# Optimization experiments

Hardware: AMD Instinct MI355X
Metric: run time of the kernel (lower is better)

Reference implementation:

```python
import jax, jax.numpy as jnp
import numpy as np

B = 16384
D_IN, HID = 4, 128
N1, N2, N3 = 32, 8, 128   # capsule counts: 32 -> 8 -> 128
D_COV, D_CAP = 1, 4
N_ITERS = 3
EPS = 1e-5


def heinsen_routing(a_inp, mu_inp, W, Bb, beta_use, beta_ign):
    """Heinsen (2019) capsule routing.
    a_inp: [b, n_inp] activations; mu_inp: [b, n_inp, d_cov, d_inp] capsules.
    W: [n_inp or 1, n_out, d_inp, d_out]; Bb: [n_out, d_cov, d_out];
    beta_use/beta_ign: [n_out].
    """
    n_inp = a_inp.shape[1]
    W = jnp.broadcast_to(W, (n_inp,) + W.shape[1:])
    n_out = W.shape[1]
    # votes V: [b, n_inp, n_out, d_cov, d_out]
    V = jnp.einsum('ijdh,bicd->bijch', W, mu_inp) + Bb
    f_a = jax.nn.sigmoid(a_inp)[..., None]  # [b, n_inp, 1]
    a_out = mu_out = sig2_out = None
    for it in range(N_ITERS):
        if it == 0:
            R = jnp.full(V.shape[:3], 1.0 / n_out, V.dtype)
        else:
            diff2 = (V - mu_out[:, None]) ** 2
            log_p = (-0.5 * diff2 / sig2_out[:, None]
                     - 0.5 * jnp.log(2.0 * np.pi * sig2_out[:, None])).sum((-2, -1))
            R = jax.nn.softmax(jax.nn.log_sigmoid(a_out)[:, None, :] + log_p, axis=-1)
        D_use = f_a * R                       # [b, n_inp, n_out]
        D_ign = f_a - D_use
        a_out = beta_use * D_use.sum(1) - beta_ign * D_ign.sum(1)  # [b, n_out]
        inv = 1.0 / (D_use.sum(1) + EPS)
        mu_out = jnp.einsum('bij,bijch->bjch', D_use, V) * inv[..., None, None]
        sig2_out = jnp.einsum('bij,bijch->bjch', D_use, (V - mu_out[:, None]) ** 2) * inv[..., None, None] + EPS
    return a_out, mu_out, sig2_out


def setup_inputs() -> dict:
    key = jax.random.key(0)
    ks = jax.random.split(key, 16)
    rn = lambda k, s, sc=1.0: (jax.random.normal(k, s) * sc).astype(jnp.float32)
    inp = rn(ks[0], (B, D_IN))
    W1 = rn(ks[1], (HID, D_IN), 1.0 / np.sqrt(D_IN)); b1 = jnp.zeros((HID,), jnp.float32)
    Wa = rn(ks[2], (HID, HID), 1.0 / np.sqrt(HID)); ba = jnp.zeros((HID,), jnp.float32)
    Wv = rn(ks[3], (N1, HID), 1.0 / np.sqrt(HID)); bv = jnp.zeros((N1,), jnp.float32)
    R1_W = rn(ks[4], (1, N2, D_CAP, D_CAP), 1.0 / D_CAP)   # n_inp not fixed -> shared W
    R1_B = rn(ks[5], (N2, D_COV, D_CAP), 0.1)
    R1_bu = rn(ks[6], (N2,), 0.1); R1_bi = rn(ks[7], (N2,), 0.1)
    R2_W = rn(ks[8], (N2, N3, D_CAP, D_CAP), 1.0 / D_CAP)
    R2_B = rn(ks[9], (N3, D_COV, D_CAP), 0.1)
    R2_bu = rn(ks[10], (N3,), 0.1); R2_bi = rn(ks[11], (N3,), 0.1)
    sub_w = rn(ks[12], (2, D_IN))  # SubNetwork weight, 2 actions x 4 input feats
    return dict(inp=inp, W1=W1, b1=b1, Wa=Wa, ba=ba, Wv=Wv, bv=bv,
                R1_W=R1_W, R1_B=R1_B, R1_bu=R1_bu, R1_bi=R1_bi,
                R2_W=R2_W, R2_B=R2_B, R2_bu=R2_bu, R2_bi=R2_bi, sub_w=sub_w)


def reference(inp, W1, b1, Wa, ba, Wv, bv, R1_W, R1_B, R1_bu, R1_bi,
              R2_W, R2_B, R2_bu, R2_bi, sub_w):
    x = jax.nn.relu(inp @ W1.T + b1)                                  # [B,128]
    action_caps = (x @ Wa.T + ba).reshape(-1, N1, D_COV, D_CAP)        # [B,32,1,4]
    state_caps = x @ Wv.T + bv                                         # [B,32]
    a, mu, _ = heinsen_routing(state_caps, action_caps, R1_W, R1_B, R1_bu, R1_bi)
    a, mu, _ = heinsen_routing(a, mu, R2_W, R2_B, R2_bu, R2_bi)        # [B,128], [B,128,1,4]
    value = a.max(axis=1)                                              # critic value [B]
    idx = jnp.argmax(a, axis=1)                                        # [B]
    sel = jnp.take_along_axis(mu, idx[:, None, None, None], axis=1)[:, 0, 0, :]  # [B,4]
    action_prob = jax.nn.softmax(sel, axis=-1)
    k1, k2, k3 = jax.random.split(jax.random.key(42), 3)
    sub_action = jax.random.categorical(k1, jnp.log(action_prob + 1e-20), axis=-1)  # [B]
    eps = jax.random.normal(k2, (inp.shape[0],) + sub_w.shape)          # [B,2,4]
    new_w = jnp.clip(jnp.where(sub_action[:, None, None] == 0, sub_w * eps, sub_w / eps), -1.0, 1.0)
    final = jnp.einsum('bi,boi->bo', inp, new_w)                       # [B,2]
    out_probs = jax.nn.softmax(final, axis=-1)
    action = jax.random.categorical(k3, jnp.log(out_probs + 1e-20), axis=-1)  # [B]
    log_prob = jnp.take_along_axis(jnp.log(out_probs + 1e-20), action[:, None], axis=1)[:, 0]
    return action, log_prob, value
```

## Files before the change

kernel.cpp:

```cpp
#include <hip/hip_runtime.h>
#include <cstdint>

#define BB 16384
#define EPSR 1e-5f
#define TWO_PI 6.2831855f

struct U2 { uint32_t x, y; };

__host__ __device__ constexpr uint32_t rotl32(uint32_t x, int r) {
  return (x << r) | (x >> (32 - r));
}

__host__ __device__ constexpr U2 tf2x32(uint32_t k0, uint32_t k1, uint32_t x0, uint32_t x1) {
  uint32_t ks0 = k0, ks1 = k1, ks2 = k0 ^ k1 ^ 0x1BD11BDAu;
  x0 += ks0; x1 += ks1;
  x0 += x1; x1 = rotl32(x1, 13); x1 ^= x0;
  x0 += x1; x1 = rotl32(x1, 15); x1 ^= x0;
  x0 += x1; x1 = rotl32(x1, 26); x1 ^= x0;
  x0 += x1; x1 = rotl32(x1, 6);  x1 ^= x0;
  x0 += ks1; x1 += ks2 + 1u;
  x0 += x1; x1 = rotl32(x1, 17); x1 ^= x0;
  x0 += x1; x1 = rotl32(x1, 29); x1 ^= x0;
  x0 += x1; x1 = rotl32(x1, 16); x1 ^= x0;
  x0 += x1; x1 = rotl32(x1, 24); x1 ^= x0;
  x0 += ks2; x1 += ks0 + 2u;
  x0 += x1; x1 = rotl32(x1, 13); x1 ^= x0;
  x0 += x1; x1 = rotl32(x1, 15); x1 ^= x0;
  x0 += x1; x1 = rotl32(x1, 26); x1 ^= x0;
  x0 += x1; x1 = rotl32(x1, 6);  x1 ^= x0;
  x0 += ks0; x1 += ks1 + 3u;
  x0 += x1; x1 = rotl32(x1, 17); x1 ^= x0;
  x0 += x1; x1 = rotl32(x1, 29); x1 ^= x0;
  x0 += x1; x1 = rotl32(x1, 16); x1 ^= x0;
  x0 += x1; x1 = rotl32(x1, 24); x1 ^= x0;
  x0 += ks1; x1 += ks2 + 4u;
  x0 += x1; x1 = rotl32(x1, 13); x1 ^= x0;
  x0 += x1; x1 = rotl32(x1, 15); x1 ^= x0;
  x0 += x1; x1 = rotl32(x1, 26); x1 ^= x0;
  x0 += x1; x1 = rotl32(x1, 6);  x1 ^= x0;
  x0 += ks2; x1 += ks0 + 5u;
  return U2{x0, x1};
}

static_assert(tf2x32(0u, 0u, 0u, 2u).x == 4146024105u, "threefry KAT A.x");
static_assert(tf2x32(0u, 0u, 0u, 2u).y == 2718843009u, "threefry KAT A.y");
static_assert(tf2x32(0u, 0u, 1u, 3u).x == 967050713u,  "threefry KAT B.x");
static_assert(tf2x32(0u, 0u, 1u, 3u).y == 1272950319u, "threefry KAT B.y");

constexpr U2 KK1 = tf2x32(0u, 42u, 0u, 0u);
constexpr U2 KK2 = tf2x32(0u, 42u, 0u, 1u);
constexpr U2 KK3 = tf2x32(0u, 42u, 0u, 2u);

__device__ __forceinline__ uint32_t rbits(uint32_t ka, uint32_t kb, uint32_t n) {
  U2 r = tf2x32(ka, kb, 0u, n);
  return r.x ^ r.y;
}

__device__ __forceinline__ float u01f(uint32_t bits) {
  return __uint_as_float((bits >> 9) | 0x3F800000u) - 1.0f;
}

__device__ __forceinline__ float gumbel_from(uint32_t bits) {
  #pragma clang fp contract(off)
  const float tiny = 1.17549435e-38f;
  float f = u01f(bits);
  float u = f * 1.0f + tiny;
  u = fmaxf(tiny, u);
  return -logf(-logf(u));
}

__device__ __forceinline__ float normal_from(uint32_t bits) {
  #pragma clang fp contract(off)
  const float lo = -0.99999994f;
  float f = u01f(bits);
  float u = f * 2.0f + lo;
  u = fmaxf(lo, u);
  float w = -log1pf(-(u * u));
  float p;
  if (w < 5.0f) {
    w = w - 2.5f;
    p = 2.81022636e-08f;
    p = 3.43273939e-07f  + p * w;
    p = -3.5233877e-06f  + p * w;
    p = -4.39150654e-06f + p * w;
    p = 0.00021858087f   + p * w;
    p = -0.00125372503f  + p * w;
    p = -0.00417768164f  + p * w;
    p = 0.246640727f     + p * w;
    p = 1.50140941f      + p * w;
  } else {
    w = sqrtf(w) - 3.0f;
    p = -0.000200214257f;
    p = 0.000100950558f  + p * w;
    p = 0.00134934322f   + p * w;
    p = -0.00367342844f  + p * w;
    p = 0.00573950773f   + p * w;
    p = -0.0076224613f   + p * w;
    p = 0.00943887047f   + p * w;
    p = 1.00167406f      + p * w;
    p = 2.83297682f      + p * w;
  }
  return 1.41421356f * (p * u);
}

__device__ __forceinline__ float frcp(float x)  { return __builtin_amdgcn_rcpf(x); }
__device__ __forceinline__ float fexp(float x)  { return __expf(x); }
__device__ __forceinline__ float flog(float x)  { return __logf(x); }
__device__ __forceinline__ float fsig(float x)  { return frcp(1.0f + fexp(-x)); }
__device__ __forceinline__ float flogsig(float x) {
  return fminf(x, 0.0f) - flog(1.0f + fexp(-fabsf(x)));
}

template<int CTRL>
__device__ __forceinline__ float fdpp(float x) {
  return __int_as_float(__builtin_amdgcn_update_dpp(
      0, __float_as_int(x), CTRL, 0xF, 0xF, true));
}
template<int CTRL>
__device__ __forceinline__ int idpp(int x) {
  return __builtin_amdgcn_update_dpp(0, x, CTRL, 0xF, 0xF, true);
}
__device__ __forceinline__ float fswz16(float x) {
  return __int_as_float(__builtin_amdgcn_ds_swizzle(__float_as_int(x), 0x401F));
}
__device__ __forceinline__ int iswz16(int x) {
  return __builtin_amdgcn_ds_swizzle(x, 0x401F);
}

__device__ __forceinline__ float redh_sum(float x) {
  x += fdpp<0xB1>(x);
  x += fdpp<0x4E>(x);
  return x;
}
__device__ __forceinline__ float red8j_sum(float x) {
  x += fdpp<0x124>(x);
  x += fdpp<0x128>(x);
  x += fswz16(x);
  return x;
}
__device__ __forceinline__ float red64_sum(float x) {
  x += fdpp<0xB1>(x);
  x += fdpp<0x4E>(x);
  x += fdpp<0x124>(x);
  x += fdpp<0x128>(x);
  x += fswz16(x);
  x += __shfl_xor(x, 32);
  return x;
}

__global__ __launch_bounds__(256) void feat_kernel(
    const float* __restrict__ inp, const float* __restrict__ W1, const float* __restrict__ b1,
    const float* __restrict__ Wa, const float* __restrict__ ba,
    const float* __restrict__ Wv, const float* __restrict__ bv,
    float* __restrict__ feat) {
  __shared__ float xs[16][129];
  const int t = threadIdx.x;
  const int bl = t & 15;
  const int og = t >> 4;
  const int b = blockIdx.x * 16 + bl;
  const float4 in4 = *reinterpret_cast<const float4*>(inp + b * 4);
  #pragma unroll
  for (int kk = 0; kk < 8; ++kk) {
    int k = og * 8 + kk;
    float s = in4.x * W1[k * 4 + 0] + in4.y * W1[k * 4 + 1] +
              in4.z * W1[k * 4 + 2] + in4.w * W1[k * 4 + 3];
    s += b1[k];
    xs[bl][k] = fmaxf(s, 0.0f);
  }
  __syncthreads();
  #pragma unroll
  for (int pass = 0; pass < 2; ++pass) {
    const int o0 = og * 10 + pass * 5;
    const float* rr0; const float* rr1; const float* rr2;
    const float* rr3; const float* rr4;
    float bs[5];
    {
      int oo = o0 + 0; rr0 = (oo < 128) ? Wa + oo * 128 : Wv + (oo - 128) * 128;
      bs[0] = (oo < 128) ? ba[oo] : bv[oo - 128];
      oo = o0 + 1; rr1 = (oo < 128) ? Wa + oo * 128 : Wv + (oo - 128) * 128;
      bs[1] = (oo < 128) ? ba[oo] : bv[oo - 128];
      oo = o0 + 2; rr2 = (oo < 128) ? Wa + oo * 128 : Wv + (oo - 128) * 128;
      bs[2] = (oo < 128) ? ba[oo] : bv[oo - 128];
      oo = o0 + 3; rr3 = (oo < 128) ? Wa + oo * 128 : Wv + (oo - 128) * 128;
      bs[3] = (oo < 128) ? ba[oo] : bv[oo - 128];
      oo = o0 + 4; rr4 = (oo < 128) ? Wa + oo * 128 : Wv + (oo - 128) * 128;
      bs[4] = (oo < 128) ? ba[oo] : bv[oo - 128];
    }
    float s0 = 0.f, s1 = 0.f, s2 = 0.f, s3 = 0.f, s4 = 0.f;
    #pragma unroll 8
    for (int k = 0; k < 128; ++k) {
      float xv = xs[bl][k];
      s0 += rr0[k] * xv;
      s1 += rr1[k] * xv;
      s2 += rr2[k] * xv;
      s3 += rr3[k] * xv;
      s4 += rr4[k] * xv;
    }
    float* fo = feat + b * 160 + o0;
    fo[0] = s0 + bs[0]; fo[1] = s1 + bs[1]; fo[2] = s2 + bs[2];
    fo[3] = s3 + bs[3]; fo[4] = s4 + bs[4];
  }
}

__global__ __launch_bounds__(128, 4) void route_kernel(
    const float* __restrict__ feat,
    const float* __restrict__ R1W, const float* __restrict__ R1B,
    const float* __restrict__ R1bu, const float* __restrict__ R1bi,
    const float* __restrict__ R2W, const float* __restrict__ R2B,
    const float* __restrict__ R2bu, const float* __restrict__ R2bi,
    const float* __restrict__ inp, const float* __restrict__ sub_w,
    float* __restrict__ out) {
  const int lane = threadIdx.x & 63;
  const int w = threadIdx.x >> 6;
  const int b = blockIdx.x;
  const float* fb = feat + b * 160;

  __shared__ float4 r1a[3][2][32];
  __shared__ float  r1g[2][2][32];
  __shared__ float  exS[2][2][8];
  __shared__ float s_av[2];
  __shared__ int   s_ai[2];
  __shared__ float s_mu[2][4];

  const int c = lane & 31;
  const int ihalf = lane >> 5;
  const int q = w * 2 + ihalf;
  const int j1 = c >> 2, h1 = c & 3;
  const float w1r0 = R1W[(j1 * 4 + 0) * 4 + h1];
  const float w1r1 = R1W[(j1 * 4 + 1) * 4 + h1];
  const float w1r2 = R1W[(j1 * 4 + 2) * 4 + h1];
  const float w1r3 = R1W[(j1 * 4 + 3) * 4 + h1];
  const float bc1 = R1B[j1 * 4 + h1];
  const float bu1 = R1bu[j1], bi1 = R1bi[j1];

  const float sfm = fsig(fb[128 + w * 16 + (lane & 15)]);

  float v1[8], f0[8];
  #pragma unroll
  for (int ii = 0; ii < 8; ++ii) {
    int i = q * 8 + ii;
    float4 m = *reinterpret_cast<const float4*>(fb + i * 4);
    v1[ii] = w1r0 * m.x + w1r1 * m.y + w1r2 * m.z + w1r3 * m.w + bc1;
    f0[ii] = __shfl(sfm, ihalf * 8 + ii);
  }

  float a1, mu1, sig1;
  {
    float S = 0.f, Sg = 0.f, num = 0.f;
    #pragma unroll
    for (int ii = 0; ii < 8; ++ii) {
      float D = f0[ii] * 0.125f;
      S += D;
      Sg += (f0[ii] - D);
      num += D * v1[ii];
    }
    S += __shfl_xor(S, 32); Sg += __shfl_xor(Sg, 32); num += __shfl_xor(num, 32);
    if (lane < 32) r1a[0][w][c] = make_float4(S, Sg, num, 0.f);
    __syncthreads();
    float4 o = r1a[0][w ^ 1][c];
    S += o.x; Sg += o.y; num += o.z;
    a1 = bu1 * S - bi1 * Sg;
    float inv = frcp(S + EPSR);
    mu1 = num * inv;
    float sg = 0.f;
    #pragma unroll
    for (int ii = 0; ii < 8; ++ii) {
      float D = f0[ii] * 0.125f;
      float tt = v1[ii] - mu1;
      sg += D * (tt * tt);
    }
    sg += __shfl_xor(sg, 32);
    if (lane < 32) r1g[0][w][c] = sg;
    __syncthreads();
    sg += r1g[0][w ^ 1][c];
    sig1 = sg * inv + EPSR;
  }
  #pragma unroll
  for (int it = 1; it < 3; ++it) {
    const bool needsig = (it == 1);
    float lsig = flogsig(a1);
    float lt1 = -(0.5f * flog(TWO_PI * sig1));
    float nhis = -0.5f * frcp(sig1);
    float Darr[8];
    float S = 0.f, Sg = 0.f, num = 0.f;
    #pragma unroll
    for (int ii = 0; ii < 8; ++ii) {
      float tt = v1[ii] - mu1;
      float lp = (tt * tt) * nhis + lt1;
      lp = redh_sum(lp);
      float logit = lsig + lp;
      float e = fexp(logit);
      float den = red8j_sum(e);
      float D = f0[ii] * (e * frcp(den));
      Darr[ii] = D;
      S += D;
      Sg += (f0[ii] - D);
      num += D * v1[ii];
    }
    S += __shfl_xor(S, 32); Sg += __shfl_xor(Sg, 32); num += __shfl_xor(num, 32);
    if (lane < 32) r1a[it][w][c] = make_float4(S, Sg, num, 0.f);
    __syncthreads();
    float4 o = r1a[it][w ^ 1][c];
    S += o.x; Sg += o.y; num += o.z;
    a1 = bu1 * S - bi1 * Sg;
    float inv = frcp(S + EPSR);
    mu1 = num * inv;
    if (needsig) {
      float sg = 0.f;
      #pragma unroll
      for (int ii = 0; ii < 8; ++ii) {
        float tt = v1[ii] - mu1;
        sg += Darr[ii] * (tt * tt);
      }
      sg += __shfl_xor(sg, 32);
      if (lane < 32) r1g[1][w][c] = sg;
      __syncthreads();
      sg += r1g[1][w ^ 1][c];
      sig1 = sg * inv + EPSR;
    }
  }

  const float sa = fsig(__shfl(a1, (lane & 7) * 4));
  float f1[8];
  #pragma unroll
  for (int i = 0; i < 8; ++i) f1[i] = __shfl(sa, i);

  const int j = w * 64 + lane;
  const float4 b4 = *reinterpret_cast<const float4*>(R2B + j * 4);
  const float bb2[4] = {b4.x, b4.y, b4.z, b4.w};
  const float bu2 = R2bu[j], bi2 = R2bi[j];

  float v2[8][4];
  #pragma unroll
  for (int i = 0; i < 8; ++i) {
    float m0 = __shfl(mu1, i * 4 + 0);
    float m1 = __shfl(mu1, i * 4 + 1);
    float m2 = __shfl(mu1, i * 4 + 2);
    float m3 = __shfl(mu1, i * 4 + 3);
    const float4* wp = reinterpret_cast<const float4*>(R2W + i * 2048 + j * 16);
    float4 c0 = wp[0], c1 = wp[1], c2 = wp[2], c3 = wp[3];
    v2[i][0] = m0 * c0.x + m1 * c1.x + m2 * c2.x + m3 * c3.x + bb2[0];
    v2[i][1] = m0 * c0.y + m1 * c1.y + m2 * c2.y + m3 * c3.y + bb2[1];
    v2[i][2] = m0 * c0.z + m1 * c1.z + m2 * c2.z + m3 * c3.z + bb2[2];
    v2[i][3] = m0 * c0.w + m1 * c1.w + m2 * c2.w + m3 * c3.w + bb2[3];
  }

  float a2, mu[4], sg[4];
  {
    float S = 0.f, Sg = 0.f;
    #pragma unroll
    for (int i = 0; i < 8; ++i) {
      float D = f1[i] * 0.0078125f;
      S += D;
      Sg += (f1[i] - D);
    }
    a2 = bu2 * S - bi2 * Sg;
    float inv = frcp(S + EPSR);
    #pragma unroll
    for (int h = 0; h < 4; ++h) {
      float n = 0.f;
      #pragma unroll
      for (int i = 0; i < 8; ++i) n += (f1[i] * 0.0078125f) * v2[i][h];
      mu[h] = n * inv;
    }
    #pragma unroll
    for (int h = 0; h < 4; ++h) {
      float s2 = 0.f;
      #pragma unroll
      for (int i = 0; i < 8; ++i) {
        float D = f1[i] * 0.0078125f;
        float t = v2[i][h] - mu[h];
        s2 += D * (t * t);
      }
      sg[h] = s2 * inv + EPSR;
    }
  }

  float e[8], stw[8];
  #pragma unroll
  for (int it = 1; it < 3; ++it) {
    const bool needsig = (it == 1);
    float lsig = flogsig(a2);
    float lt[4], is[4];
    #pragma unroll
    for (int h = 0; h < 4; ++h) {
      lt[h] = -(0.5f * flog(TWO_PI * sg[h]));
      is[h] = -0.5f * frcp(sg[h]);
    }
    #pragma unroll
    for (int i = 0; i < 8; ++i) {
      float lp = 0.f;
      #pragma unroll
      for (int h = 0; h < 4; ++h) {
        float t = v2[i][h] - mu[h];
        lp += (t * t) * is[h] + lt[h];
      }
      float l = lsig + lp;
      e[i] = fexp(l);
      stw[i] = red64_sum(e[i]);
    }
    if (lane == 0) {
      #pragma unroll
      for (int i = 0; i < 8; ++i) exS[it - 1][w][i] = stw[i];
    }
    __syncthreads();
    float D[8];
    float SA = 0.f, SgS = 0.f;
    float n[4] = {0.f, 0.f, 0.f, 0.f};
    #pragma unroll
    for (int i = 0; i < 8; ++i) {
      float Stot = stw[i] + exS[it - 1][w ^ 1][i];
      float Dv = f1[i] * (e[i] * frcp(Stot));
      D[i] = Dv;
      SA += Dv;
      SgS += (f1[i] - Dv);
      #pragma unroll
      for (int h = 0; h < 4; ++h) n[h] += Dv * v2[i][h];
    }
    a2 = bu2 * SA - bi2 * SgS;
    float inv = frcp(SA + EPSR);
    #pragma unroll
    for (int h = 0; h < 4; ++h) mu[h] = n[h] * inv;
    if (needsig) {
      #pragma unroll
      for (int h = 0; h < 4; ++h) {
        float s2 = 0.f;
        #pragma unroll
        for (int i = 0; i < 8; ++i) {
          float t = v2[i][h] - mu[h];
          s2 += D[i] * (t * t);
        }
        sg[h] = s2 * inv + EPSR;
      }
    }
  }

  float bv = a2; int bj = j;
  {
    float ov; int oj;
    ov = fdpp<0xB1>(bv);  oj = idpp<0xB1>(bj);
    if (ov > bv || (ov == bv && oj < bj)) { bv = ov; bj = oj; }
    ov = fdpp<0x4E>(bv);  oj = idpp<0x4E>(bj);
    if (ov > bv || (ov == bv && oj < bj)) { bv = ov; bj = oj; }
    ov = fdpp<0x124>(bv); oj = idpp<0x124>(bj);
    if (ov > bv || (ov == bv && oj < bj)) { bv = ov; bj = oj; }
    ov = fdpp<0x128>(bv); oj = idpp<0x128>(bj);
    if (ov > bv || (ov == bv && oj < bj)) { bv = ov; bj = oj; }
    ov = fswz16(bv);      oj = iswz16(bj);
    if (ov > bv || (ov == bv && oj < bj)) { bv = ov; bj = oj; }
    ov = __shfl_xor(bv, 32); oj = __shfl_xor(bj, 32);
    if (ov > bv || (ov == bv && oj < bj)) { bv = ov; bj = oj; }
  }
  if (lane == 0) { s_av[w] = bv; s_ai[w] = bj; }
  if (j == bj) {
    s_mu[w][0] = mu[0]; s_mu[w][1] = mu[1]; s_mu[w][2] = mu[2]; s_mu[w][3] = mu[3];
  }
  __syncthreads();

  if (w == 0) {
    float av0 = s_av[0], av1 = s_av[1];
    float value; int winw;
    if (av1 > av0) { value = av1; winw = 1; }
    else           { value = av0; winw = 0; }
    float sel[4] = {s_mu[winw][0], s_mu[winw][1], s_mu[winw][2], s_mu[winw][3]};

    float gu, no;
    {
      uint32_t ka, kb, nn;
      if (lane < 4)       { ka = KK1.x; kb = KK1.y; nn = (uint32_t)(b * 4 + lane); }
      else if (lane < 12) { ka = KK2.x; kb = KK2.y; nn = (uint32_t)(b * 8 + (lane - 4)); }
      else                { ka = KK3.x; kb = KK3.y; nn = (uint32_t)(b * 2 + (lane & 1)); }
      uint32_t bits = rbits(ka, kb, nn);
      gu = gumbel_from(bits);
      no = normal_from(bits);
    }
    const float g0 = __shfl(gu, 0), g1 = __shfl(gu, 1);
    const float g2 = __shfl(gu, 2), g3 = __shfl(gu, 3);
    float ep[8];
    #pragma unroll
    for (int i = 0; i < 8; ++i) ep[i] = __shfl(no, 4 + i);
    const float q0 = __shfl(gu, 12), q1 = __shfl(gu, 13);

    float mx = fmaxf(fmaxf(sel[0], sel[1]), fmaxf(sel[2], sel[3]));
    float ex[4], sesum = 0.f;
    #pragma unroll
    for (int cc = 0; cc < 4; ++cc) { ex[cc] = fexp(sel[cc] - mx); sesum += ex[cc]; }
    float rs0 = frcp(sesum);
    float lg1[4];
    #pragma unroll
    for (int cc = 0; cc < 4; ++cc) lg1[cc] = flog(ex[cc] * rs0 + 1e-20f);

    float sc0 = g0 + lg1[0], sc1 = g1 + lg1[1];
    float sc2 = g2 + lg1[2], sc3 = g3 + lg1[3];
    int sub_action = 0;
    float bestsc = sc0;
    if (sc1 > bestsc) { bestsc = sc1; sub_action = 1; }
    if (sc2 > bestsc) { bestsc = sc2; sub_action = 2; }
    if (sc3 > bestsc) { bestsc = sc3; sub_action = 3; }

    float4 ib4 = *reinterpret_cast<const float4*>(inp + b * 4);
    float inb[4] = {ib4.x, ib4.y, ib4.z, ib4.w};
    float fin[2];
    #pragma unroll
    for (int o = 0; o < 2; ++o) {
      float acc = 0.f;
      #pragma unroll
      for (int i2 = 0; i2 < 4; ++i2) {
        float eps = ep[o * 4 + i2];
        float sw = sub_w[o * 4 + i2];
        float nw = (sub_action == 0) ? sw * eps : sw / eps;
        nw = fminf(fmaxf(nw, -1.0f), 1.0f);
        acc += inb[i2] * nw;
      }
      fin[o] = acc;
    }

    float mx2 = fmaxf(fin[0], fin[1]);
    float e0 = fexp(fin[0] - mx2), e1 = fexp(fin[1] - mx2);
    float rsum = frcp(e0 + e1);
    float lgp0 = flog(e0 * rsum + 1e-20f);
    float lgp1 = flog(e1 * rsum + 1e-20f);
    float s0 = q0 + lgp0;
    float s1 = q1 + lgp1;
    int action = (s1 > s0) ? 1 : 0;
    float log_prob = action ? lgp1 : lgp0;

    if (lane == 0) {
      out[b] = (float)action;
      out[BB + b] = log_prob;
      out[2 * BB + b] = value;
    }
  }
}

extern "C" void kernel_launch(void* const* d_in, const int* in_sizes, int n_in,
                              void* d_out, int out_size, void* d_ws, size_t ws_size,
                              hipStream_t stream) {
  const float* inp  = (const float*)d_in[0];
  const float* W1   = (const float*)d_in[1];
  const float* b1   = (const float*)d_in[2];
  const float* Wa   = (const float*)d_in[3];
  const float* ba   = (const float*)d_in[4];
  const float* Wv   = (const float*)d_in[5];
  const float* bv   = (const float*)d_in[6];
  const float* R1W  = (const float*)d_in[7];
  const float* R1B  = (const float*)d_in[8];
  const float* R1bu = (const float*)d_in[9];
  const float* R1bi = (const float*)d_in[10];
  const float* R2W  = (const float*)d_in[11];
  const float* R2B  = (const float*)d_in[12];
  const float* R2bu = (const float*)d_in[13];
  const float* R2bi = (const float*)d_in[14];
  const float* sub_w= (const float*)d_in[15];
  float* out = (float*)d_out;
  float* feat = (float*)d_ws;

  feat_kernel<<<BB / 16, 256, 0, stream>>>(inp, W1, b1, Wa, ba, Wv, bv, feat);
  route_kernel<<<BB, 128, 0, stream>>>(feat, R1W, R1B, R1bu, R1bi,
                                       R2W, R2B, R2bu, R2bi, inp, sub_w, out);
}
```

Baseline: 163.6 us.

## Retile feature kernel, fold log-prob constants into exp2, stage mu via LDS

The feature kernel now handles 64 batch rows per block, with a wave-uniform output group and the 160 outputs split across 4 blocks. This is meant to reuse each weight-row load across more rows, at the cost of recomputing the first layer in every quarter block. In both routing stages the per-dimension log-normal constants and log-sigmoid are folded into a single pre-scaled constant, and exp is swapped for a raw exp2 to trim VALU work. The stage-2 broadcast of mu1 and the sigmoid activations now goes through shared memory with float4 reads instead of many shuffles, which adds one extra barrier.

```diff
diff --git a/kernel.cpp b/kernel.cpp
--- a/kernel.cpp
+++ b/kernel.cpp
@@ -4,6 +4,7 @@
 #define BB 16384
 #define EPSR 1e-5f
 #define TWO_PI 6.2831855f
+#define L2E 1.44269504f
 
 struct U2 { uint32_t x, y; };
 
@@ -106,6 +107,13 @@
 __device__ __forceinline__ float frcp(float x)  { return __builtin_amdgcn_rcpf(x); }
 __device__ __forceinline__ float fexp(float x)  { return __expf(x); }
 __device__ __forceinline__ float flog(float x)  { return __logf(x); }
+__device__ __forceinline__ float fexp2(float x) {
+#if __has_builtin(__builtin_amdgcn_exp2f)
+  return __builtin_amdgcn_exp2f(x);
+#else
+  return __expf(x * 0.69314718f);
+#endif
+}
 __device__ __forceinline__ float fsig(float x)  { return frcp(1.0f + fexp(-x)); }
 __device__ __forceinline__ float flogsig(float x) {
   return fminf(x, 0.0f) - flog(1.0f + fexp(-fabsf(x)));
@@ -153,15 +161,17 @@
     const float* __restrict__ Wa, const float* __restrict__ ba,
     const float* __restrict__ Wv, const float* __restrict__ bv,
     float* __restrict__ feat) {
-  __shared__ float xs[16][129];
+  __shared__ float xs[64][129];
   const int t = threadIdx.x;
-  const int bl = t & 15;
-  const int og = t >> 4;
-  const int b = blockIdx.x * 16 + bl;
+  const int bl = t & 63;
+  const int og = __builtin_amdgcn_readfirstlane(t >> 6);
+  const int btile = blockIdx.x >> 2;
+  const int qtr = blockIdx.x & 3;
+  const int b = btile * 64 + bl;
   const float4 in4 = *reinterpret_cast<const float4*>(inp + b * 4);
   #pragma unroll
-  for (int kk = 0; kk < 8; ++kk) {
-    int k = og * 8 + kk;
+  for (int jj = 0; jj < 32; ++jj) {
+    int k = og * 32 + jj;
     float s = in4.x * W1[k * 4 + 0] + in4.y * W1[k * 4 + 1] +
               in4.z * W1[k * 4 + 2] + in4.w * W1[k * 4 + 3];
     s += b1[k];
@@ -170,7 +180,7 @@
   __syncthreads();
   #pragma unroll
   for (int pass = 0; pass < 2; ++pass) {
-    const int o0 = og * 10 + pass * 5;
+    const int o0 = qtr * 40 + og * 10 + pass * 5;
     const float* rr0; const float* rr1; const float* rr2;
     const float* rr3; const float* rr4;
     float bs[5];
@@ -218,6 +228,8 @@
   __shared__ float4 r1a[3][2][32];
   __shared__ float  r1g[2][2][32];
   __shared__ float  exS[2][2][8];
+  __shared__ __align__(16) float s_mu1[32];
+  __shared__ __align__(16) float s_f1[8];
   __shared__ float s_av[2];
   __shared__ int   s_ai[2];
   __shared__ float s_mu[2][4];
@@ -280,16 +292,17 @@
     const bool needsig = (it == 1);
     float lsig = flogsig(a1);
     float lt1 = -(0.5f * flog(TWO_PI * sig1));
-    float nhis = -0.5f * frcp(sig1);
+    float ltq = redh_sum(lt1);
+    float C2 = (lsig + ltq) * L2E;
+    float nhis2 = (-0.5f * L2E) * frcp(sig1);
     float Darr[8];
     float S = 0.f, Sg = 0.f, num = 0.f;
     #pragma unroll
     for (int ii = 0; ii < 8; ++ii) {
       float tt = v1[ii] - mu1;
-      float lp = (tt * tt) * nhis + lt1;
+      float lp = (tt * tt) * nhis2;
       lp = redh_sum(lp);
-      float logit = lsig + lp;
-      float e = fexp(logit);
+      float e = fexp2(lp + C2);
       float den = red8j_sum(e);
       float D = f0[ii] * (e * frcp(den));
       Darr[ii] = D;
@@ -320,10 +333,18 @@
     }
   }
 
-  const float sa = fsig(__shfl(a1, (lane & 7) * 4));
+  if (w == 0 && lane < 32) {
+    s_mu1[c] = mu1;
+    if (h1 == 0) s_f1[j1] = fsig(a1);
+  }
+  __syncthreads();
   float f1[8];
-  #pragma unroll
-  for (int i = 0; i < 8; ++i) f1[i] = __shfl(sa, i);
+  {
+    float4 fa = *reinterpret_cast<const float4*>(&s_f1[0]);
+    float4 fbq = *reinterpret_cast<const float4*>(&s_f1[4]);
+    f1[0] = fa.x; f1[1] = fa.y; f1[2] = fa.z; f1[3] = fa.w;
+    f1[4] = fbq.x; f1[5] = fbq.y; f1[6] = fbq.z; f1[7] = fbq.w;
+  }
 
   const int j = w * 64 + lane;
   const float4 b4 = *reinterpret_cast<const float4*>(R2B + j * 4);
@@ -333,16 +354,13 @@
   float v2[8][4];
   #pragma unroll
   for (int i = 0; i < 8; ++i) {
-    float m0 = __shfl(mu1, i * 4 + 0);
-    float m1 = __shfl(mu1, i * 4 + 1);
-    float m2 = __shfl(mu1, i * 4 + 2);
-    float m3 = __shfl(mu1, i * 4 + 3);
+    float4 mu4 = *reinterpret_cast<const float4*>(&s_mu1[i * 4]);
     const float4* wp = reinterpret_cast<const float4*>(R2W + i * 2048 + j * 16);
     float4 c0 = wp[0], c1 = wp[1], c2 = wp[2], c3 = wp[3];
-    v2[i][0] = m0 * c0.x + m1 * c1.x + m2 * c2.x + m3 * c3.x + bb2[0];
-    v2[i][1] = m0 * c0.y + m1 * c1.y + m2 * c2.y + m3 * c3.y + bb2[1];
-    v2[i][2] = m0 * c0.z + m1 * c1.z + m2 * c2.z + m3 * c3.z + bb2[2];
-    v2[i][3] = m0 * c0.w + m1 * c1.w + m2 * c2.w + m3 * c3.w + bb2[3];
+    v2[i][0] = mu4.x * c0.x + mu4.y * c1.x + mu4.z * c2.x + mu4.w * c3.x + bb2[0];
+    v2[i][1] = mu4.x * c0.y + mu4.y * c1.y + mu4.z * c2.y + mu4.w * c3.y + bb2[1];
+    v2[i][2] = mu4.x * c0.z + mu4.y * c1.z + mu4.z * c2.z + mu4.w * c3.z + bb2[2];
+    v2[i][3] = mu4.x * c0.w + mu4.y * c1.w + mu4.z * c2.w + mu4.w * c3.w + bb2[3];
   }
 
   float a2, mu[4], sg[4];
@@ -381,22 +399,22 @@
   for (int it = 1; it < 3; ++it) {
     const bool needsig = (it == 1);
     float lsig = flogsig(a2);
-    float lt[4], is[4];
+    float is2[4], ltS = 0.f;
     #pragma unroll
     for (int h = 0; h < 4; ++h) {
-      lt[h] = -(0.5f * flog(TWO_PI * sg[h]));
-      is[h] = -0.5f * frcp(sg[h]);
-    }
+      ltS += -(0.5f * flog(TWO_PI * sg[h]));
+      is2[h] = (-0.5f * L2E) * frcp(sg[h]);
+    }
+    const float C2 = (lsig + ltS) * L2E;
     #pragma unroll
     for (int i = 0; i < 8; ++i) {
-      float lp = 0.f;
+      float lp = C2;
       #pragma unroll
       for (int h = 0; h < 4; ++h) {
         float t = v2[i][h] - mu[h];
-        lp += (t * t) * is[h] + lt[h];
+        lp = fmaf(t * t, is2[h], lp);
       }
-      float l = lsig + lp;
-      e[i] = fexp(l);
+      e[i] = fexp2(lp);
       stw[i] = red64_sum(e[i]);
     }
     if (lane == 0) {
@@ -555,7 +573,7 @@
   float* out = (float*)d_out;
   float* feat = (float*)d_ws;
 
-  feat_kernel<<<BB / 16, 256, 0, stream>>>(inp, W1, b1, Wa, ba, Wv, bv, feat);
+  feat_kernel<<<(BB / 64) * 4, 256, 0, stream>>>(inp, W1, b1, Wa, ba, Wv, bv, feat);
   route_kernel<<<BB, 128, 0, stream>>>(feat, R1W, R1B, R1bu, R1bi,
                                        R2W, R2B, R2bu, R2bi, inp, sub_w, out);
 }
```

Measured after the change: 140.9 us. 13.9% less time.
